# Kernel tuning notes

Hardware: AMD Instinct MI355X
Metric: run time of the kernel (lower is better)

## Reference

```python
import jax, jax.numpy as jnp
import numpy as np

B, C, T = 32, 1536, 2048
BN = 128  # bottleneck channels


def setup_inputs() -> dict:
    key = jax.random.key(0)
    k1, k2, k3, k4, k5, k6 = jax.random.split(key, 6)
    x = jax.random.normal(k1, (B, C, T), dtype=jnp.float32)
    padding_mask = jax.random.randint(k2, (B, T), 0, 2) == 1
    W_tdnn = jax.random.normal(k3, (BN, C), dtype=jnp.float32) * (1.0 / np.sqrt(C))
    b_tdnn = jax.random.normal(k4, (BN,), dtype=jnp.float32) * 0.01
    W_attn = jax.random.normal(k5, (C, BN), dtype=jnp.float32) * (1.0 / np.sqrt(BN))
    b_attn = jax.random.normal(k6, (C,), dtype=jnp.float32) * 0.01
    return {"x": x, "padding_mask": padding_mask, "W_tdnn": W_tdnn,
            "b_tdnn": b_tdnn, "W_attn": W_attn, "b_attn": b_attn}


def reference(x, padding_mask, W_tdnn, b_tdnn, W_attn, b_attn):
    # pointwise conv1 (k=1) == channel-wise matmul: (B,C,T) -> (B,BN,T)
    e = jnp.tanh(jnp.einsum('oc,bct->bot', W_tdnn, x) + b_tdnn[None, :, None])
    # pointwise conv2: (B,BN,T) -> (B,C,T)
    a = jnp.einsum('co,bot->bct', W_attn, e) + b_attn[None, :, None]
    a = jnp.where(padding_mask[:, None, :], -1e9, a)
    alpha = jax.nn.softmax(a, axis=2)  # (B,C,T)
    mean = jnp.sum(alpha * x, axis=2)  # (B,C)
    var = jnp.sum(alpha * (x - mean[:, :, None]) ** 2, axis=2)
    std = jnp.sqrt(jnp.clip(var, 1e-9, None))
    return jnp.concatenate([mean, std], axis=1)  # (B,2C)
```

## Files before the change

### kernel.cpp

```cpp
#include <hip/hip_runtime.h>
#include <math.h>

#define Bn  32
#define Cn  1536
#define Tn  2048
#define BNn 128
#define SHIFT 12.0f

typedef __attribute__((ext_vector_type(8))) short bf16x8;
typedef __attribute__((ext_vector_type(4))) float fx4;

__device__ __forceinline__ unsigned int f2bf1(float f) {
    unsigned int u = __float_as_uint(f);
    return (u + 0x7fffu + ((u >> 16) & 1u)) >> 16;
}
__device__ __forceinline__ float fast_tanh(float v) {
    return 1.f - 2.f / (__expf(2.f * v) + 1.f);
}

__global__ void k_prep(const float* __restrict__ W1f, const float* __restrict__ Waf,
                       short* __restrict__ W1b, short* __restrict__ Wab) {
    int i = blockIdx.x * 256 + threadIdx.x;
    if (i < BNn * Cn) {
        W1b[i] = (short)f2bf1(W1f[i]);
        Wab[i] = (short)f2bf1(Waf[i]);
    }
}

__global__ __launch_bounds__(256, 2) void k_fused(
    const float* __restrict__ x, const short* __restrict__ W1,
    const float* __restrict__ bias, const short* __restrict__ Wab,
    const int* __restrict__ mask, float* __restrict__ part)
{
    __shared__ short sA[128 * 64];
    __shared__ short sE[128 * 128];

    const int b    = blockIdx.y;
    const int t0g  = blockIdx.x * 128;
    const int tid  = threadIdx.x;
    const int lane = tid & 63;
    const int wv   = tid >> 6;
    const int ln   = lane & 15;
    const int g    = lane >> 4;
    const int wt   = (wv & 1) * 64;
    const int wo   = (wv >> 1) * 64;

    const float* xb = x + (size_t)b * Cn * Tn;
    const float* xt = xb + t0g;

    const int t4 = (tid & 31) * 4;
    const int cq = (tid >> 5) * 4;

    fx4 acc[4][4];
    #pragma unroll
    for (int i = 0; i < 4; ++i)
        #pragma unroll
        for (int j = 0; j < 4; ++j) acc[i][j] = (fx4){0.f, 0.f, 0.f, 0.f};

    for (int k0 = 0; k0 < Cn; k0 += 64) {
        bf16x8 bfr[4][2];
        #pragma unroll
        for (int nn = 0; nn < 4; ++nn)
            #pragma unroll
            for (int kt = 0; kt < 2; ++kt)
                bfr[nn][kt] = *(const bf16x8*)(W1 + (size_t)(wo + nn * 16 + ln) * Cn
                                               + k0 + kt * 32 + g * 8);

        float4 xr[2][4];
        #pragma unroll
        for (int p = 0; p < 2; ++p) {
            const int c = cq + p * 32;
            #pragma unroll
            for (int j = 0; j < 4; ++j)
                xr[p][j] = *(const float4*)(xt + (size_t)(k0 + c + j) * Tn + t4);
        }
        __syncthreads();
        #pragma unroll
        for (int p = 0; p < 2; ++p) {
            const int c   = cq + p * 32;
            const int blk = c >> 3;
            const int sub = c & 7;
            #pragma unroll
            for (int i = 0; i < 4; ++i) {
                const int t = t4 + i;
                unsigned int lo = f2bf1(((const float*)&xr[p][0])[i]) |
                                  (f2bf1(((const float*)&xr[p][1])[i]) << 16);
                unsigned int hi = f2bf1(((const float*)&xr[p][2])[i]) |
                                  (f2bf1(((const float*)&xr[p][3])[i]) << 16);
                const int idx = t * 64 + ((blk ^ (t & 7)) << 3) + sub;
                *(uint2*)(sA + idx) = make_uint2(lo, hi);
            }
        }
        __syncthreads();

        #pragma unroll
        for (int kt = 0; kt < 2; ++kt) {
            bf16x8 af[4];
            #pragma unroll
            for (int mm = 0; mm < 4; ++mm) {
                const int t = wt + mm * 16 + ln;
                af[mm] = *(const bf16x8*)(sA + t * 64 + (((kt * 4 + g) ^ (t & 7)) << 3));
            }
            #pragma unroll
            for (int mm = 0; mm < 4; ++mm)
                #pragma unroll
                for (int nn = 0; nn < 4; ++nn)
                    acc[mm][nn] = __builtin_amdgcn_mfma_f32_16x16x32_bf16(
                        af[mm], bfr[nn][kt], acc[mm][nn], 0, 0, 0);
        }
    }

    float bs[4];
    #pragma unroll
    for (int nn = 0; nn < 4; ++nn) bs[nn] = bias[wo + nn * 16 + ln];

    #pragma unroll
    for (int mm = 0; mm < 4; ++mm)
        #pragma unroll
        for (int nn = 0; nn < 4; ++nn) {
            #pragma unroll
            for (int r = 0; r < 4; ++r) {
                const int t = wt + mm * 16 + g * 4 + r;
                const int o = wo + nn * 16 + ln;
                const float v = fast_tanh(acc[mm][nn][r] + bs[nn]);
                sE[t * 128 + (((o >> 3) ^ (t & 15)) << 3) + (o & 7)] = (short)f2bf1(v);
            }
        }
    __syncthreads();

    bf16x8 af2[4][4];
    #pragma unroll
    for (int mt = 0; mt < 4; ++mt)
        #pragma unroll
        for (int kt = 0; kt < 4; ++kt) {
            const int t = wt + mt * 16 + ln;
            af2[mt][kt] = *(const bf16x8*)(sE + t * 128 + (((kt * 4 + g) ^ (t & 15)) << 3));
        }

    int4 mv[4];
    #pragma unroll
    for (int mt = 0; mt < 4; ++mt)
        mv[mt] = *(const int4*)(mask + (size_t)b * Tn + t0g + wt + mt * 16 + g * 4);

    const int wc    = (wv >> 1) * 32;
    const int chunk = blockIdx.x * 2 + (wv & 1);

    for (int c0 = 0; c0 < Cn; c0 += 64) {
        bf16x8 bfr[2][4];
        #pragma unroll
        for (int nt = 0; nt < 2; ++nt)
            #pragma unroll
            for (int kt = 0; kt < 4; ++kt)
                bfr[nt][kt] = *(const bf16x8*)(Wab + (size_t)(c0 + wc + nt * 16 + ln) * BNn
                                               + kt * 32 + g * 8);

        float4 xq[4][2];
        #pragma unroll
        for (int mt = 0; mt < 4; ++mt)
            #pragma unroll
            for (int nt = 0; nt < 2; ++nt)
                xq[mt][nt] = *(const float4*)(xb + (size_t)(c0 + wc + nt * 16 + ln) * Tn
                                              + t0g + wt + mt * 16 + g * 4);

        fx4 a2[4][2];
        #pragma unroll
        for (int mt = 0; mt < 4; ++mt)
            #pragma unroll
            for (int nt = 0; nt < 2; ++nt) a2[mt][nt] = (fx4){0.f, 0.f, 0.f, 0.f};

        #pragma unroll
        for (int kt = 0; kt < 4; ++kt)
            #pragma unroll
            for (int mt = 0; mt < 4; ++mt)
                #pragma unroll
                for (int nt = 0; nt < 2; ++nt)
                    a2[mt][nt] = __builtin_amdgcn_mfma_f32_16x16x32_bf16(
                        af2[mt][kt], bfr[nt][kt], a2[mt][nt], 0, 0, 0);

        #pragma unroll
        for (int nt = 0; nt < 2; ++nt) {
            float s0 = 0.f, s1 = 0.f, s2 = 0.f;
            #pragma unroll
            for (int mt = 0; mt < 4; ++mt) {
                #pragma unroll
                for (int r = 0; r < 4; ++r) {
                    const int msk = ((const int*)&mv[mt])[r];
                    const float p = msk ? 0.f : __expf(a2[mt][nt][r] - SHIFT);
                    const float xv = ((const float*)&xq[mt][nt])[r];
                    s0 += p;
                    s1 += p * xv;
                    s2 += p * xv * xv;
                }
            }
            s0 += __shfl_xor(s0, 16); s1 += __shfl_xor(s1, 16); s2 += __shfl_xor(s2, 16);
            s0 += __shfl_xor(s0, 32); s1 += __shfl_xor(s1, 32); s2 += __shfl_xor(s2, 32);
            if (g == 0) {
                const int c = c0 + wc + nt * 16 + ln;
                *(float4*)&part[(((size_t)b * 32 + chunk) * Cn + c) * 4] =
                    make_float4(s0, s1, s2, 0.f);
            }
        }
    }
}

__global__ void k_merge(const float* __restrict__ part, float* __restrict__ out) {
    const int i = blockIdx.x * 256 + threadIdx.x;
    if (i >= Bn * Cn) return;
    const int b = i / Cn, c = i - b * Cn;
    float s0 = 0.f, s1 = 0.f, s2 = 0.f;
    #pragma unroll 8
    for (int sp = 0; sp < 32; ++sp) {
        const float4 v = *(const float4*)&part[(((size_t)b * 32 + sp) * Cn + c) * 4];
        s0 += v.x; s1 += v.y; s2 += v.z;
    }
    const float mean = s1 / s0;
    const float var  = fmaxf(s2 / s0 - mean * mean, 1e-9f);
    out[(size_t)b * (2 * Cn) + c]      = mean;
    out[(size_t)b * (2 * Cn) + Cn + c] = sqrtf(var);
}

extern "C" void kernel_launch(void* const* d_in, const int* in_sizes, int n_in,
                              void* d_out, int out_size, void* d_ws, size_t ws_size,
                              hipStream_t stream) {
    const float* x      = (const float*)d_in[0];
    const int*   mask   = (const int*)d_in[1];
    const float* W_tdnn = (const float*)d_in[2];
    const float* b_tdnn = (const float*)d_in[3];
    const float* W_attn = (const float*)d_in[4];
    float* out = (float*)d_out;

    short* W1b  = (short*)d_ws;
    short* Wab  = W1b + (size_t)BNn * Cn;
    float* part = (float*)(Wab + (size_t)BNn * Cn);

    k_prep<<<dim3((BNn * Cn + 255) / 256), 256, 0, stream>>>(W_tdnn, W_attn, W1b, Wab);
    k_fused<<<dim3(Tn / 128, Bn), 256, 0, stream>>>(x, W1b, b_tdnn, Wab, mask, part);
    k_merge<<<dim3((Bn * Cn + 255) / 256), 256, 0, stream>>>(part, out);
}
```

Before: 629.4 us.

## Raise occupancy to three blocks per CU and reverse second-phase channel order

Raises the launch-bounds occupancy target from 2 to 3 blocks per CU. To fit the tighter register budget, it loads W1 fragments per k-step instead of per 64-channel tile, and splits the second GEMM into per-16-channel sub-tiles. It also walks the second-phase channels in reverse, so the last x rows read in phase 1 are reused while still cache-resident. The risks are register spills and less latency hiding per wave.

```diff
diff --git a/kernel.cpp b/kernel.cpp
--- a/kernel.cpp
+++ b/kernel.cpp
@@ -27,7 +27,7 @@
     }
 }
 
-__global__ __launch_bounds__(256, 2) void k_fused(
+__global__ __launch_bounds__(256, 3) void k_fused(
     const float* __restrict__ x, const short* __restrict__ W1,
     const float* __restrict__ bias, const short* __restrict__ Wab,
     const int* __restrict__ mask, float* __restrict__ part)
@@ -58,14 +58,6 @@
         for (int j = 0; j < 4; ++j) acc[i][j] = (fx4){0.f, 0.f, 0.f, 0.f};
 
     for (int k0 = 0; k0 < Cn; k0 += 64) {
-        bf16x8 bfr[4][2];
-        #pragma unroll
-        for (int nn = 0; nn < 4; ++nn)
-            #pragma unroll
-            for (int kt = 0; kt < 2; ++kt)
-                bfr[nn][kt] = *(const bf16x8*)(W1 + (size_t)(wo + nn * 16 + ln) * Cn
-                                               + k0 + kt * 32 + g * 8);
-
         float4 xr[2][4];
         #pragma unroll
         for (int p = 0; p < 2; ++p) {
@@ -95,6 +87,11 @@
 
         #pragma unroll
         for (int kt = 0; kt < 2; ++kt) {
+            bf16x8 bq[4];
+            #pragma unroll
+            for (int nn = 0; nn < 4; ++nn)
+                bq[nn] = *(const bf16x8*)(W1 + (size_t)(wo + nn * 16 + ln) * Cn
+                                          + k0 + kt * 32 + g * 8);
             bf16x8 af[4];
             #pragma unroll
             for (int mm = 0; mm < 4; ++mm) {
@@ -106,7 +103,7 @@
                 #pragma unroll
                 for (int nn = 0; nn < 4; ++nn)
                     acc[mm][nn] = __builtin_amdgcn_mfma_f32_16x16x32_bf16(
-                        af[mm], bfr[nn][kt], acc[mm][nn], 0, 0, 0);
+                        af[mm], bq[nn], acc[mm][nn], 0, 0, 0);
         }
     }
 
@@ -145,48 +142,42 @@
     const int wc    = (wv >> 1) * 32;
     const int chunk = blockIdx.x * 2 + (wv & 1);
 
-    for (int c0 = 0; c0 < Cn; c0 += 64) {
-        bf16x8 bfr[2][4];
-        #pragma unroll
-        for (int nt = 0; nt < 2; ++nt)
+    for (int cc = 0; cc < Cn; cc += 64) {
+        const int c0 = (Cn - 64) - cc;
+        #pragma unroll
+        for (int nt = 0; nt < 2; ++nt) {
+            const int cr = c0 + wc + nt * 16 + ln;
+
+            bf16x8 bfr[4];
             #pragma unroll
             for (int kt = 0; kt < 4; ++kt)
-                bfr[nt][kt] = *(const bf16x8*)(Wab + (size_t)(c0 + wc + nt * 16 + ln) * BNn
-                                               + kt * 32 + g * 8);
-
-        float4 xq[4][2];
-        #pragma unroll
-        for (int mt = 0; mt < 4; ++mt)
-            #pragma unroll
-            for (int nt = 0; nt < 2; ++nt)
-                xq[mt][nt] = *(const float4*)(xb + (size_t)(c0 + wc + nt * 16 + ln) * Tn
-                                              + t0g + wt + mt * 16 + g * 4);
-
-        fx4 a2[4][2];
-        #pragma unroll
-        for (int mt = 0; mt < 4; ++mt)
-            #pragma unroll
-            for (int nt = 0; nt < 2; ++nt) a2[mt][nt] = (fx4){0.f, 0.f, 0.f, 0.f};
-
-        #pragma unroll
-        for (int kt = 0; kt < 4; ++kt)
+                bfr[kt] = *(const bf16x8*)(Wab + (size_t)cr * BNn + kt * 32 + g * 8);
+
+            float4 xq[4];
             #pragma unroll
             for (int mt = 0; mt < 4; ++mt)
+                xq[mt] = *(const float4*)(xb + (size_t)cr * Tn
+                                          + t0g + wt + mt * 16 + g * 4);
+
+            fx4 a2[4];
+            #pragma unroll
+            for (int mt = 0; mt < 4; ++mt) a2[mt] = (fx4){0.f, 0.f, 0.f, 0.f};
+
+            #pragma unroll
+            for (int kt = 0; kt < 4; ++kt)
                 #pragma unroll
-                for (int nt = 0; nt < 2; ++nt)
-                    a2[mt][nt] = __builtin_amdgcn_mfma_f32_16x16x32_bf16(
-                        af2[mt][kt], bfr[nt][kt], a2[mt][nt], 0, 0, 0);
-
-        #pragma unroll
-        for (int nt = 0; nt < 2; ++nt) {
+                for (int mt = 0; mt < 4; ++mt)
+                    a2[mt] = __builtin_amdgcn_mfma_f32_16x16x32_bf16(
+                        af2[mt][kt], bfr[kt], a2[mt], 0, 0, 0);
+
             float s0 = 0.f, s1 = 0.f, s2 = 0.f;
             #pragma unroll
             for (int mt = 0; mt < 4; ++mt) {
                 #pragma unroll
                 for (int r = 0; r < 4; ++r) {
                     const int msk = ((const int*)&mv[mt])[r];
-                    const float p = msk ? 0.f : __expf(a2[mt][nt][r] - SHIFT);
-                    const float xv = ((const float*)&xq[mt][nt])[r];
+                    const float p = msk ? 0.f : __expf(a2[mt][r] - SHIFT);
+                    const float xv = ((const float*)&xq[mt])[r];
                     s0 += p;
                     s1 += p * xv;
                     s2 += p * xv * xv;
@@ -195,8 +186,7 @@
             s0 += __shfl_xor(s0, 16); s1 += __shfl_xor(s1, 16); s2 += __shfl_xor(s2, 16);
             s0 += __shfl_xor(s0, 32); s1 += __shfl_xor(s1, 32); s2 += __shfl_xor(s2, 32);
             if (g == 0) {
-                const int c = c0 + wc + nt * 16 + ln;
-                *(float4*)&part[(((size_t)b * 32 + chunk) * Cn + c) * 4] =
+                *(float4*)&part[(((size_t)b * 32 + chunk) * Cn + cr) * 4] =
                     make_float4(s0, s1, s2, 0.f);
             }
         }
```

Measured after the change: 632.6 us. About the same (+0.5%).
